# Optimization experiments

Hardware: AMD Instinct MI355X
Metric: run time of the kernel (lower is better)

Reference implementation:

```python
import jax, jax.numpy as jnp
import numpy as np

HEADS = 8
DIM_HEAD = 64
SCALE = DIM_HEAD ** -0.5


def setup_inputs() -> dict:
    key = jax.random.key(0)
    ks = jax.random.split(key, 5)
    B, N, M, D = 8, 1024, 1024, 512
    inner = HEADS * DIM_HEAD  # 512
    return {
        "x": jax.random.normal(ks[0], (B, N, D), dtype=jnp.float32),
        "context": jax.random.normal(ks[1], (B, M, D), dtype=jnp.float32),
        "Wq": jax.random.normal(ks[2], (D, inner), dtype=jnp.float32) * (D ** -0.5),
        "Wkv": jax.random.normal(ks[3], (D, 2 * inner), dtype=jnp.float32) * (D ** -0.5),
        "Wo": jax.random.normal(ks[4], (inner, D), dtype=jnp.float32) * (inner ** -0.5),
        "bo": jnp.zeros((D,), dtype=jnp.float32),
    }


def reference(x, context, Wq, Wkv, Wo, bo):
    B, N, D = x.shape
    M = context.shape[1]
    q = x @ Wq                      # [B, N, inner]
    kv = context @ Wkv              # [B, M, 2*inner]
    k, v = jnp.split(kv, 2, axis=-1)
    # b n (h d) -> b h n d
    split_heads = lambda t: t.reshape(t.shape[0], t.shape[1], HEADS, DIM_HEAD).transpose(0, 2, 1, 3)
    q, k, v = split_heads(q), split_heads(k), split_heads(v)
    dots = jnp.einsum('bhid,bhjd->bhij', q, k) * SCALE  # [B, H, N, M]
    attn = jax.nn.softmax(dots, axis=-1)
    out = jnp.einsum('bhij,bhjd->bhid', attn, v)        # [B, H, N, d]
    out = out.transpose(0, 2, 1, 3).reshape(B, N, HEADS * DIM_HEAD)
    return out @ Wo + bo            # [B, N, D]
```

## Files before the change

### kernel.cpp

```cpp
#include <hip/hip_runtime.h>
#include <stdint.h>

#define LOG2E 1.44269504088896340736f
#define QSCALE (0.125f * LOG2E)

typedef __bf16 bf16x8 __attribute__((ext_vector_type(8)));
typedef float floatx4 __attribute__((ext_vector_type(4)));

__device__ __forceinline__ unsigned short bfbits(float f) {
  __bf16 h = (__bf16)f;
  return __builtin_bit_cast(unsigned short, h);
}

__device__ __forceinline__ float fast_exp2(float x) {
#if __has_builtin(__builtin_amdgcn_exp2f)
  return __builtin_amdgcn_exp2f(x);
#else
  return exp2f(x);
#endif
}

__device__ __forceinline__ void gl2lds16(const void* g, void* l) {
  __builtin_amdgcn_global_load_lds((const __attribute__((address_space(1))) void*)g,
                                   (__attribute__((address_space(3))) void*)l, 16, 0, 0);
}

__global__ __launch_bounds__(256) void cvt2_f32_bf16(const float* __restrict__ a,
                                                     const float* __restrict__ b,
                                                     unsigned short* __restrict__ oa,
                                                     unsigned short* __restrict__ ob) {
  int blk = blockIdx.x;
  const float* in = blk < 4096 ? a : b;
  unsigned short* out = blk < 4096 ? oa : ob;
  int i = (((blk & 4095) * 256) + threadIdx.x) * 4;
  float4 v = *(const float4*)(in + i);
  unsigned long long pk = (unsigned long long)bfbits(v.x)
                        | ((unsigned long long)bfbits(v.y) << 16)
                        | ((unsigned long long)bfbits(v.z) << 32)
                        | ((unsigned long long)bfbits(v.w) << 48);
  *(unsigned long long*)(out + i) = pk;
}

__global__ __launch_bounds__(256) void transpose_cvt3(const float* __restrict__ w0,
                                                      const float* __restrict__ w1,
                                                      const float* __restrict__ w2,
                                                      unsigned short* __restrict__ o0,
                                                      unsigned short* __restrict__ o1,
                                                      unsigned short* __restrict__ o2) {
  __shared__ float tile[32][33];
  int z = blockIdx.z;
  const float* in = (z == 0) ? w0 : ((z == 1) ? w1 : w2);
  unsigned short* out = (z == 0) ? o0 : ((z == 1) ? o1 : o2);
  const int N = (z == 1) ? 1024 : 512;
  if (blockIdx.x * 32 >= N) return;
  const int K = 512;
  int k0 = blockIdx.y * 32, n0 = blockIdx.x * 32;
#pragma unroll
  for (int r = threadIdx.y; r < 32; r += 8)
    tile[r][threadIdx.x] = in[(long)(k0 + r) * N + n0 + threadIdx.x];
  __syncthreads();
#pragma unroll
  for (int r = threadIdx.y; r < 32; r += 8)
    out[(long)(n0 + r) * K + k0 + threadIdx.x] = bfbits(tile[threadIdx.x][r]);
}

template <int EPI, int BM>
__global__ __launch_bounds__(256)
void gemm_bf16(const unsigned short* __restrict__ A,
               const unsigned short* __restrict__ Bt,
               unsigned short* __restrict__ outA,
               unsigned short* __restrict__ outB,
               float* __restrict__ outF,
               const float* __restrict__ bias,
               int M, int N, int K)
{
  constexpr int IC = BM / 32;
  __shared__ unsigned short As[BM * 32];
  __shared__ unsigned short Bs[128 * 32];

  const int tid = threadIdx.x;
  const int wave = tid >> 6;
  const int lane = tid & 63;
  const int l15 = lane & 15;
  const int q4 = lane >> 4;
  const int wm = (wave & 1) * (BM / 2);
  const int wn = (wave >> 1) * 64;
  const long bm = (long)blockIdx.y * BM;
  const long bn = (long)blockIdx.x * 128;

  floatx4 acc[IC][4];
#pragma unroll
  for (int i = 0; i < IC; ++i)
#pragma unroll
    for (int j = 0; j < 4; ++j) { acc[i][j][0]=0.f; acc[i][j][1]=0.f; acc[i][j][2]=0.f; acc[i][j][3]=0.f; }

  for (int k0 = 0; k0 < K; k0 += 32) {
#pragma unroll
    for (int cc = 0; cc < BM / 64; ++cc) {
      int c = cc * 256 + tid;
      int r = c >> 2, kc = c & 3;
      gl2lds16(A + (bm + r) * (long)K + k0 + kc * 8, (char*)As + c * 16);
    }
#pragma unroll
    for (int cc = 0; cc < 2; ++cc) {
      int c = cc * 256 + tid;
      int r = c >> 2, kc = c & 3;
      gl2lds16(Bt + (bn + r) * (long)K + k0 + kc * 8, (char*)Bs + c * 16);
    }
    __syncthreads();
    bf16x8 af[IC], bfr[4];
#pragma unroll
    for (int i = 0; i < IC; ++i)
      af[i] = *(const bf16x8*)(As + (wm + i * 16 + l15) * 32 + q4 * 8);
#pragma unroll
    for (int j = 0; j < 4; ++j)
      bfr[j] = *(const bf16x8*)(Bs + (wn + j * 16 + l15) * 32 + q4 * 8);
#pragma unroll
    for (int i = 0; i < IC; ++i)
#pragma unroll
      for (int j = 0; j < 4; ++j)
        acc[i][j] = __builtin_amdgcn_mfma_f32_16x16x32_bf16(af[i], bfr[j], acc[i][j], 0, 0, 0);
    __syncthreads();
  }

#pragma unroll
  for (int i = 0; i < IC; ++i) {
#pragma unroll
    for (int j = 0; j < 4; ++j) {
      long col = bn + wn + j * 16 + l15;
      if (EPI == 1 && bn >= 512) {
        long h = (col - 512) >> 6, d = col & 63;
        long row0 = bm + wm + i * 16 + q4 * 4;
        long b = row0 >> 10, m0 = row0 & 1023;
        unsigned long long pk = (unsigned long long)bfbits(acc[i][j][0])
                              | ((unsigned long long)bfbits(acc[i][j][1]) << 16)
                              | ((unsigned long long)bfbits(acc[i][j][2]) << 32)
                              | ((unsigned long long)bfbits(acc[i][j][3]) << 48);
        *(unsigned long long*)(outB + ((b * 8 + h) * 64 + d) * 1024 + m0) = pk;
      } else {
#pragma unroll
        for (int r = 0; r < 4; ++r) {
          long row = bm + wm + i * 16 + q4 * 4 + r;
          float v = acc[i][j][r];
          if (EPI == 0) {
            long b = row >> 10, n = row & 1023;
            long h = col >> 6, d = col & 63;
            outA[((b * 8 + h) * 1024 + n) * 64 + d] = bfbits(v * QSCALE);
          } else if (EPI == 1) {
            long b = row >> 10, m = row & 1023;
            long h = col >> 6, d = col & 63;
            outA[((b * 8 + h) * 1024 + m) * 64 + d] = bfbits(v);
          } else {
            outF[row * (long)N + col] = v + bias[col];
          }
        }
      }
    }
  }
}

__global__ __launch_bounds__(256)
void attn_kernel(const unsigned short* __restrict__ Qb,
                 const unsigned short* __restrict__ Kb,
                 const unsigned short* __restrict__ Vt,
                 unsigned short* __restrict__ Ob)
{
  __shared__ unsigned short Ksm[2][4096];
  __shared__ unsigned short Vsm[2][4096];
  __shared__ unsigned short Psm[128 * 64];

  const int tid = threadIdx.x;
  const int wave = tid >> 6;
  const int lane = tid & 63;
  const int l15 = lane & 15;
  const int q4 = lane >> 4;
  const int bh = blockIdx.x;
  const int nb = blockIdx.y;

  const long qrow0 = (long)bh * 1024 + nb * 128 + wave * 32;

  bf16x8 qf[2][2];
#pragma unroll
  for (int i = 0; i < 2; ++i)
#pragma unroll
    for (int ks = 0; ks < 2; ++ks)
      qf[i][ks] = *(const bf16x8*)(Qb + (qrow0 + i * 16 + l15) * 64 + ks * 32 + q4 * 8);

  floatx4 acc[2][4];
#pragma unroll
  for (int i = 0; i < 2; ++i)
#pragma unroll
    for (int d = 0; d < 4; ++d) { acc[i][d][0]=0.f; acc[i][d][1]=0.f; acc[i][d][2]=0.f; acc[i][d][3]=0.f; }
  float suml[2][4];
#pragma unroll
  for (int i = 0; i < 2; ++i)
#pragma unroll
    for (int r = 0; r < 4; ++r) suml[i][r] = 0.0f;

  const unsigned short* Kbase = Kb + (long)bh * 65536;
  const unsigned short* Vbase = Vt + (long)bh * 65536;
  int koff[2], voff[2], lds16[2];
#pragma unroll
  for (int cc = 0; cc < 2; ++cc) {
    int c = cc * 256 + tid;
    int jrow = c >> 3;
    int cact = (c & 7) ^ (jrow & 7);
    koff[cc] = jrow * 64 + cact * 8;
    voff[cc] = jrow * 1024 + cact * 8;
    lds16[cc] = c * 16;
  }

#pragma unroll
  for (int cc = 0; cc < 2; ++cc) {
    gl2lds16(Kbase + koff[cc], (char*)Ksm[0] + lds16[cc]);
    gl2lds16(Vbase + voff[cc], (char*)Vsm[0] + lds16[cc]);
  }

  for (int t = 0; t < 16; ++t) {
    __syncthreads();
    const int cur = t & 1;
    if (t + 1 < 16) {
      const int nxt = cur ^ 1;
#pragma unroll
      for (int cc = 0; cc < 2; ++cc) {
        gl2lds16(Kbase + (t + 1) * 4096 + koff[cc], (char*)Ksm[nxt] + lds16[cc]);
        gl2lds16(Vbase + (t + 1) * 64 + voff[cc], (char*)Vsm[nxt] + lds16[cc]);
      }
    }

    floatx4 s[2][4];
#pragma unroll
    for (int i = 0; i < 2; ++i)
#pragma unroll
      for (int j = 0; j < 4; ++j) { s[i][j][0]=0.f; s[i][j][1]=0.f; s[i][j][2]=0.f; s[i][j][3]=0.f; }
#pragma unroll
    for (int ks = 0; ks < 2; ++ks) {
      bf16x8 kfr[4];
#pragma unroll
      for (int jn = 0; jn < 4; ++jn) {
        int j = jn * 16 + l15;
        int cact = (ks * 4 + q4) ^ (j & 7);
        kfr[jn] = *(const bf16x8*)(Ksm[cur] + j * 64 + cact * 8);
      }
#pragma unroll
      for (int i = 0; i < 2; ++i)
#pragma unroll
        for (int jn = 0; jn < 4; ++jn)
          s[i][jn] = __builtin_amdgcn_mfma_f32_16x16x32_bf16(qf[i][ks], kfr[jn], s[i][jn], 0, 0, 0);
    }

#pragma unroll
    for (int i = 0; i < 2; ++i) {
#pragma unroll
      for (int jn = 0; jn < 4; ++jn) {
        int colbase = jn * 16 + l15;
#pragma unroll
        for (int r = 0; r < 4; ++r) {
          float p = fast_exp2(s[i][jn][r]);
          suml[i][r] += p;
          int row = wave * 32 + i * 16 + q4 * 4 + r;
          int idx = row * 64 + (((colbase >> 3) ^ (row & 7)) << 3) + (colbase & 7);
          ((__bf16*)Psm)[idx] = (__bf16)p;
        }
      }
    }
    __asm__ volatile("s_waitcnt lgkmcnt(0)" ::: "memory");

#pragma unroll
    for (int ks = 0; ks < 2; ++ks) {
      bf16x8 pa[2], vb[4];
#pragma unroll
      for (int i = 0; i < 2; ++i) {
        int m = wave * 32 + i * 16 + l15;
        int cact = (ks * 4 + q4) ^ (m & 7);
        pa[i] = *(const bf16x8*)(Psm + m * 64 + cact * 8);
      }
#pragma unroll
      for (int dn = 0; dn < 4; ++dn) {
        int dd = dn * 16 + l15;
        int cact = (ks * 4 + q4) ^ (dd & 7);
        vb[dn] = *(const bf16x8*)(Vsm[cur] + dd * 64 + cact * 8);
      }
#pragma unroll
      for (int i = 0; i < 2; ++i)
#pragma unroll
        for (int dn = 0; dn < 4; ++dn)
          acc[i][dn] = __builtin_amdgcn_mfma_f32_16x16x32_bf16(pa[i], vb[dn], acc[i][dn], 0, 0, 0);
    }
  }

  const int b = bh >> 3, h = bh & 7;
#pragma unroll
  for (int i = 0; i < 2; ++i) {
    float inv[4];
#pragma unroll
    for (int r = 0; r < 4; ++r) {
      float l = suml[i][r];
#pragma unroll
      for (int off = 8; off >= 1; off >>= 1)
        l += __shfl_xor(l, off, 64);
      inv[r] = 1.0f / l;
    }
#pragma unroll
    for (int dn = 0; dn < 4; ++dn) {
#pragma unroll
      for (int r = 0; r < 4; ++r) {
        long row = (long)b * 1024 + nb * 128 + wave * 32 + i * 16 + q4 * 4 + r;
        long col = h * 64 + dn * 16 + l15;
        Ob[row * 512 + col] = bfbits(acc[i][dn][r] * inv[r]);
      }
    }
  }
}

extern "C" void kernel_launch(void* const* d_in, const int* in_sizes, int n_in,
                              void* d_out, int out_size, void* d_ws, size_t ws_size,
                              hipStream_t stream) {
  const float* x   = (const float*)d_in[0];
  const float* ctx = (const float*)d_in[1];
  const float* Wq  = (const float*)d_in[2];
  const float* Wkv = (const float*)d_in[3];
  const float* Wo  = (const float*)d_in[4];
  const float* bo  = (const float*)d_in[5];
  float* out = (float*)d_out;

  char* ws = (char*)d_ws;
  unsigned short* Xb   = (unsigned short*)(ws);
  unsigned short* Cb   = (unsigned short*)(ws + (8u  << 20));
  unsigned short* WqT  = (unsigned short*)(ws + (16u << 20));
  unsigned short* WkvT = (unsigned short*)(ws + (17u << 20));
  unsigned short* WoT  = (unsigned short*)(ws + (19u << 20));
  unsigned short* Qb   = (unsigned short*)(ws + (20u << 20));
  unsigned short* Kb   = (unsigned short*)(ws + (28u << 20));
  unsigned short* Vt   = (unsigned short*)(ws + (36u << 20));
  unsigned short* Ob   = (unsigned short*)(ws + (44u << 20));

  cvt2_f32_bf16<<<8192, 256, 0, stream>>>(x, ctx, Xb, Cb);
  transpose_cvt3<<<dim3(32, 16, 3), dim3(32, 8), 0, stream>>>(Wq, Wkv, Wo, WqT, WkvT, WoT);

  gemm_bf16<0, 64><<<dim3(4, 128), 256, 0, stream>>>(Xb, WqT, Qb, nullptr, nullptr, nullptr, 8192, 512, 512);
  gemm_bf16<1, 128><<<dim3(8, 64), 256, 0, stream>>>(Cb, WkvT, Kb, Vt, nullptr, nullptr, 8192, 1024, 512);
  attn_kernel<<<dim3(64, 8), 256, 0, stream>>>(Qb, Kb, Vt, Ob);
  gemm_bf16<2, 64><<<dim3(4, 128), 256, 0, stream>>>(Ob, WoT, nullptr, nullptr, out, bo, 8192, 512, 512);
}
```

Baseline: 174.0 us.

## Merge prep and projection kernels, halve attention tile, transpose S MFMA

Folds the two conversion kernels into one launch and the Q and KV projection GEMMs into one 1536-block launch, cutting launch count from six to four. The attention kernel now handles 64 query rows per block (16 per wave) and launches twice as many blocks, which gives more parallelism and less register pressure per wave. It computes S transposed (K as the A operand) so each lane holds four consecutive P values and writes them as one packed 8-byte LDS store instead of scalar bf16 stores. The row-sum reduction now needs only two shuffles plus a broadcast. In exchange, each K/V tile loaded into LDS is reused by fewer query rows, so K/V traffic per block rises.

New measurement: 162.4 us. -6.7%, faster.

```diff
diff --git a/kernel.cpp b/kernel.cpp
--- a/kernel.cpp
+++ b/kernel.cpp
@@ -25,81 +25,79 @@
                                    (__attribute__((address_space(3))) void*)l, 16, 0, 0);
 }
 
-__global__ __launch_bounds__(256) void cvt2_f32_bf16(const float* __restrict__ a,
-                                                     const float* __restrict__ b,
-                                                     unsigned short* __restrict__ oa,
-                                                     unsigned short* __restrict__ ob) {
+__global__ __launch_bounds__(256)
+void prep_kernel(const float* __restrict__ x, const float* __restrict__ ctx,
+                 const float* __restrict__ Wq, const float* __restrict__ Wkv,
+                 const float* __restrict__ Wo,
+                 unsigned short* __restrict__ Xb, unsigned short* __restrict__ Cb,
+                 unsigned short* __restrict__ WqT, unsigned short* __restrict__ WkvT,
+                 unsigned short* __restrict__ WoT) {
   int blk = blockIdx.x;
-  const float* in = blk < 4096 ? a : b;
-  unsigned short* out = blk < 4096 ? oa : ob;
-  int i = (((blk & 4095) * 256) + threadIdx.x) * 4;
-  float4 v = *(const float4*)(in + i);
-  unsigned long long pk = (unsigned long long)bfbits(v.x)
-                        | ((unsigned long long)bfbits(v.y) << 16)
-                        | ((unsigned long long)bfbits(v.z) << 32)
-                        | ((unsigned long long)bfbits(v.w) << 48);
-  *(unsigned long long*)(out + i) = pk;
-}
-
-__global__ __launch_bounds__(256) void transpose_cvt3(const float* __restrict__ w0,
-                                                      const float* __restrict__ w1,
-                                                      const float* __restrict__ w2,
-                                                      unsigned short* __restrict__ o0,
-                                                      unsigned short* __restrict__ o1,
-                                                      unsigned short* __restrict__ o2) {
-  __shared__ float tile[32][33];
-  int z = blockIdx.z;
-  const float* in = (z == 0) ? w0 : ((z == 1) ? w1 : w2);
-  unsigned short* out = (z == 0) ? o0 : ((z == 1) ? o1 : o2);
-  const int N = (z == 1) ? 1024 : 512;
-  if (blockIdx.x * 32 >= N) return;
-  const int K = 512;
-  int k0 = blockIdx.y * 32, n0 = blockIdx.x * 32;
-#pragma unroll
-  for (int r = threadIdx.y; r < 32; r += 8)
-    tile[r][threadIdx.x] = in[(long)(k0 + r) * N + n0 + threadIdx.x];
-  __syncthreads();
-#pragma unroll
-  for (int r = threadIdx.y; r < 32; r += 8)
-    out[(long)(n0 + r) * K + k0 + threadIdx.x] = bfbits(tile[threadIdx.x][r]);
-}
-
-template <int EPI, int BM>
+  int tid = threadIdx.x;
+  if (blk < 8192) {
+    const float* in = blk < 4096 ? x : ctx;
+    unsigned short* out = blk < 4096 ? Xb : Cb;
+    int i = (((blk & 4095) * 256) + tid) * 4;
+    float4 v = *(const float4*)(in + i);
+    unsigned long long pk = (unsigned long long)bfbits(v.x)
+                          | ((unsigned long long)bfbits(v.y) << 16)
+                          | ((unsigned long long)bfbits(v.z) << 32)
+                          | ((unsigned long long)bfbits(v.w) << 48);
+    *(unsigned long long*)(out + i) = pk;
+  } else {
+    __shared__ float tile[32][33];
+    int t = blk - 8192;
+    const float* in; unsigned short* out; int N; int tb;
+    if (t < 256)      { in = Wq;  out = WqT;  N = 512;  tb = t; }
+    else if (t < 768) { in = Wkv; out = WkvT; N = 1024; tb = t - 256; }
+    else              { in = Wo;  out = WoT;  N = 512;  tb = t - 768; }
+    const int K = 512;
+    int nbx = N / 32;
+    int n0 = (tb % nbx) * 32, k0 = (tb / nbx) * 32;
+    int tx = tid & 31, ty = tid >> 5;
+#pragma unroll
+    for (int r = ty; r < 32; r += 8)
+      tile[r][tx] = in[(long)(k0 + r) * N + n0 + tx];
+    __syncthreads();
+#pragma unroll
+    for (int r = ty; r < 32; r += 8)
+      out[(long)(n0 + r) * K + k0 + tx] = bfbits(tile[tx][r]);
+  }
+}
+
 __global__ __launch_bounds__(256)
-void gemm_bf16(const unsigned short* __restrict__ A,
-               const unsigned short* __restrict__ Bt,
-               unsigned short* __restrict__ outA,
-               unsigned short* __restrict__ outB,
-               float* __restrict__ outF,
-               const float* __restrict__ bias,
-               int M, int N, int K)
-{
-  constexpr int IC = BM / 32;
-  __shared__ unsigned short As[BM * 32];
+void proj_gemm(const unsigned short* __restrict__ Xb, const unsigned short* __restrict__ Cb,
+               const unsigned short* __restrict__ WqT, const unsigned short* __restrict__ WkvT,
+               unsigned short* __restrict__ Qb, unsigned short* __restrict__ Kb,
+               unsigned short* __restrict__ Vt) {
+  __shared__ unsigned short As[64 * 32];
   __shared__ unsigned short Bs[128 * 32];
+
+  int idx = blockIdx.x;
+  const unsigned short* A; const unsigned short* Bt;
+  long bm, bn; int role;
+  if (idx < 512) { role = 0; A = Xb; Bt = WqT;  bn = (long)(idx & 3) * 128; bm = (long)(idx >> 2) * 64; }
+  else { idx -= 512; role = 1; A = Cb; Bt = WkvT; bn = (long)(idx & 7) * 128; bm = (long)(idx >> 3) * 64; }
 
   const int tid = threadIdx.x;
   const int wave = tid >> 6;
   const int lane = tid & 63;
   const int l15 = lane & 15;
   const int q4 = lane >> 4;
-  const int wm = (wave & 1) * (BM / 2);
+  const int wm = (wave & 1) * 32;
   const int wn = (wave >> 1) * 64;
-  const long bm = (long)blockIdx.y * BM;
-  const long bn = (long)blockIdx.x * 128;
-
-  floatx4 acc[IC][4];
-#pragma unroll
-  for (int i = 0; i < IC; ++i)
+  const int K = 512;
+
+  floatx4 acc[2][4];
+#pragma unroll
+  for (int i = 0; i < 2; ++i)
 #pragma unroll
     for (int j = 0; j < 4; ++j) { acc[i][j][0]=0.f; acc[i][j][1]=0.f; acc[i][j][2]=0.f; acc[i][j][3]=0.f; }
 
   for (int k0 = 0; k0 < K; k0 += 32) {
-#pragma unroll
-    for (int cc = 0; cc < BM / 64; ++cc) {
-      int c = cc * 256 + tid;
-      int r = c >> 2, kc = c & 3;
-      gl2lds16(A + (bm + r) * (long)K + k0 + kc * 8, (char*)As + c * 16);
+    {
+      int r = tid >> 2, kc = tid & 3;
+      gl2lds16(A + (bm + r) * (long)K + k0 + kc * 8, (char*)As + tid * 16);
     }
 #pragma unroll
     for (int cc = 0; cc < 2; ++cc) {
@@ -108,15 +106,15 @@
       gl2lds16(Bt + (bn + r) * (long)K + k0 + kc * 8, (char*)Bs + c * 16);
     }
     __syncthreads();
-    bf16x8 af[IC], bfr[4];
-#pragma unroll
-    for (int i = 0; i < IC; ++i)
+    bf16x8 af[2], bfr[4];
+#pragma unroll
+    for (int i = 0; i < 2; ++i)
       af[i] = *(const bf16x8*)(As + (wm + i * 16 + l15) * 32 + q4 * 8);
 #pragma unroll
     for (int j = 0; j < 4; ++j)
       bfr[j] = *(const bf16x8*)(Bs + (wn + j * 16 + l15) * 32 + q4 * 8);
 #pragma unroll
-    for (int i = 0; i < IC; ++i)
+    for (int i = 0; i < 2; ++i)
 #pragma unroll
       for (int j = 0; j < 4; ++j)
         acc[i][j] = __builtin_amdgcn_mfma_f32_16x16x32_bf16(af[i], bfr[j], acc[i][j], 0, 0, 0);
@@ -124,11 +122,11 @@
   }
 
 #pragma unroll
-  for (int i = 0; i < IC; ++i) {
+  for (int i = 0; i < 2; ++i) {
 #pragma unroll
     for (int j = 0; j < 4; ++j) {
       long col = bn + wn + j * 16 + l15;
-      if (EPI == 1 && bn >= 512) {
+      if (role == 1 && col >= 512) {
         long h = (col - 512) >> 6, d = col & 63;
         long row0 = bm + wm + i * 16 + q4 * 4;
         long b = row0 >> 10, m0 = row0 & 1023;
@@ -136,23 +134,16 @@
                               | ((unsigned long long)bfbits(acc[i][j][1]) << 16)
                               | ((unsigned long long)bfbits(acc[i][j][2]) << 32)
                               | ((unsigned long long)bfbits(acc[i][j][3]) << 48);
-        *(unsigned long long*)(outB + ((b * 8 + h) * 64 + d) * 1024 + m0) = pk;
+        *(unsigned long long*)(Vt + ((b * 8 + h) * 64 + d) * 1024 + m0) = pk;
       } else {
+        long h = col >> 6, d = col & 63;
 #pragma unroll
         for (int r = 0; r < 4; ++r) {
           long row = bm + wm + i * 16 + q4 * 4 + r;
+          long b = row >> 10, n = row & 1023;
           float v = acc[i][j][r];
-          if (EPI == 0) {
-            long b = row >> 10, n = row & 1023;
-            long h = col >> 6, d = col & 63;
-            outA[((b * 8 + h) * 1024 + n) * 64 + d] = bfbits(v * QSCALE);
-          } else if (EPI == 1) {
-            long b = row >> 10, m = row & 1023;
-            long h = col >> 6, d = col & 63;
-            outA[((b * 8 + h) * 1024 + m) * 64 + d] = bfbits(v);
-          } else {
-            outF[row * (long)N + col] = v + bias[col];
-          }
+          if (role == 0) Qb[((b * 8 + h) * 1024 + n) * 64 + d] = bfbits(v * QSCALE);
+          else           Kb[((b * 8 + h) * 1024 + n) * 64 + d] = bfbits(v);
         }
       }
     }
@@ -167,7 +158,7 @@
 {
   __shared__ unsigned short Ksm[2][4096];
   __shared__ unsigned short Vsm[2][4096];
-  __shared__ unsigned short Psm[128 * 64];
+  __shared__ unsigned short Psm[64 * 64];
 
   const int tid = threadIdx.x;
   const int wave = tid >> 6;
@@ -177,25 +168,15 @@
   const int bh = blockIdx.x;
   const int nb = blockIdx.y;
 
-  const long qrow0 = (long)bh * 1024 + nb * 128 + wave * 32;
-
-  bf16x8 qf[2][2];
-#pragma unroll
-  for (int i = 0; i < 2; ++i)
-#pragma unroll
-    for (int ks = 0; ks < 2; ++ks)
-      qf[i][ks] = *(const bf16x8*)(Qb + (qrow0 + i * 16 + l15) * 64 + ks * 32 + q4 * 8);
-
-  floatx4 acc[2][4];
-#pragma unroll
-  for (int i = 0; i < 2; ++i)
-#pragma unroll
-    for (int d = 0; d < 4; ++d) { acc[i][d][0]=0.f; acc[i][d][1]=0.f; acc[i][d][2]=0.f; acc[i][d][3]=0.f; }
-  float suml[2][4];
-#pragma unroll
-  for (int i = 0; i < 2; ++i)
-#pragma unroll
-    for (int r = 0; r < 4; ++r) suml[i][r] = 0.0f;
+  bf16x8 qf[2];
+#pragma unroll
+  for (int ks = 0; ks < 2; ++ks)
+    qf[ks] = *(const bf16x8*)(Qb + ((long)bh * 1024 + nb * 64 + wave * 16 + l15) * 64 + ks * 32 + q4 * 8);
+
+  floatx4 acc[4];
+#pragma unroll
+  for (int d = 0; d < 4; ++d) { acc[d][0]=0.f; acc[d][1]=0.f; acc[d][2]=0.f; acc[d][3]=0.f; }
+  float suml = 0.0f;
 
   const unsigned short* Kbase = Kb + (long)bh * 65536;
   const unsigned short* Vbase = Vt + (long)bh * 65536;
@@ -209,13 +190,14 @@
     voff[cc] = jrow * 1024 + cact * 8;
     lds16[cc] = c * 16;
   }
-
 #pragma unroll
   for (int cc = 0; cc < 2; ++cc) {
     gl2lds16(Kbase + koff[cc], (char*)Ksm[0] + lds16[cc]);
     gl2lds16(Vbase + voff[cc], (char*)Vsm[0] + lds16[cc]);
   }
 
+  const int prow = wave * 16 + l15;
+
   for (int t = 0; t < 16; ++t) {
     __syncthreads();
     const int cur = t & 1;
@@ -228,11 +210,9 @@
       }
     }
 
-    floatx4 s[2][4];
-#pragma unroll
-    for (int i = 0; i < 2; ++i)
-#pragma unroll
-      for (int j = 0; j < 4; ++j) { s[i][j][0]=0.f; s[i][j][1]=0.f; s[i][j][2]=0.f; s[i][j][3]=0.f; }
+    floatx4 st[4];
+#pragma unroll
+    for (int jn = 0; jn < 4; ++jn) { st[jn][0]=0.f; st[jn][1]=0.f; st[jn][2]=0.f; st[jn][3]=0.f; }
 #pragma unroll
     for (int ks = 0; ks < 2; ++ks) {
       bf16x8 kfr[4];
@@ -243,38 +223,30 @@
         kfr[jn] = *(const bf16x8*)(Ksm[cur] + j * 64 + cact * 8);
       }
 #pragma unroll
-      for (int i = 0; i < 2; ++i)
-#pragma unroll
-        for (int jn = 0; jn < 4; ++jn)
-          s[i][jn] = __builtin_amdgcn_mfma_f32_16x16x32_bf16(qf[i][ks], kfr[jn], s[i][jn], 0, 0, 0);
-    }
-
-#pragma unroll
-    for (int i = 0; i < 2; ++i) {
-#pragma unroll
-      for (int jn = 0; jn < 4; ++jn) {
-        int colbase = jn * 16 + l15;
-#pragma unroll
-        for (int r = 0; r < 4; ++r) {
-          float p = fast_exp2(s[i][jn][r]);
-          suml[i][r] += p;
-          int row = wave * 32 + i * 16 + q4 * 4 + r;
-          int idx = row * 64 + (((colbase >> 3) ^ (row & 7)) << 3) + (colbase & 7);
-          ((__bf16*)Psm)[idx] = (__bf16)p;
-        }
-      }
+      for (int jn = 0; jn < 4; ++jn)
+        st[jn] = __builtin_amdgcn_mfma_f32_16x16x32_bf16(kfr[jn], qf[ks], st[jn], 0, 0, 0);
+    }
+
+#pragma unroll
+    for (int jn = 0; jn < 4; ++jn) {
+      float p0 = fast_exp2(st[jn][0]);
+      float p1 = fast_exp2(st[jn][1]);
+      float p2 = fast_exp2(st[jn][2]);
+      float p3 = fast_exp2(st[jn][3]);
+      suml += (p0 + p1) + (p2 + p3);
+      unsigned long long pk = (unsigned long long)bfbits(p0)
+                            | ((unsigned long long)bfbits(p1) << 16)
+                            | ((unsigned long long)bfbits(p2) << 32)
+                            | ((unsigned long long)bfbits(p3) << 48);
+      int ch8 = (jn * 2 + (q4 >> 1)) ^ (prow & 7);
+      *(unsigned long long*)(Psm + prow * 64 + ch8 * 8 + (q4 & 1) * 4) = pk;
     }
     __asm__ volatile("s_waitcnt lgkmcnt(0)" ::: "memory");
 
 #pragma unroll
     for (int ks = 0; ks < 2; ++ks) {
-      bf16x8 pa[2], vb[4];
-#pragma unroll
-      for (int i = 0; i < 2; ++i) {
-        int m = wave * 32 + i * 16 + l15;
-        int cact = (ks * 4 + q4) ^ (m & 7);
-        pa[i] = *(const bf16x8*)(Psm + m * 64 + cact * 8);
-      }
+      bf16x8 pa = *(const bf16x8*)(Psm + prow * 64 + (((ks * 4 + q4) ^ (prow & 7)) * 8));
+      bf16x8 vb[4];
 #pragma unroll
       for (int dn = 0; dn < 4; ++dn) {
         int dd = dn * 16 + l15;
@@ -282,32 +254,92 @@
         vb[dn] = *(const bf16x8*)(Vsm[cur] + dd * 64 + cact * 8);
       }
 #pragma unroll
-      for (int i = 0; i < 2; ++i)
-#pragma unroll
-        for (int dn = 0; dn < 4; ++dn)
-          acc[i][dn] = __builtin_amdgcn_mfma_f32_16x16x32_bf16(pa[i], vb[dn], acc[i][dn], 0, 0, 0);
-    }
-  }
+      for (int dn = 0; dn < 4; ++dn)
+        acc[dn] = __builtin_amdgcn_mfma_f32_16x16x32_bf16(pa, vb[dn], acc[dn], 0, 0, 0);
+    }
+  }
+
+  float l = suml;
+  l += __shfl_xor(l, 16, 64);
+  l += __shfl_xor(l, 32, 64);
+  float inv = 1.0f / l;
+  float invr[4];
+#pragma unroll
+  for (int r = 0; r < 4; ++r) invr[r] = __shfl(inv, q4 * 4 + r, 64);
 
   const int b = bh >> 3, h = bh & 7;
 #pragma unroll
+  for (int dn = 0; dn < 4; ++dn) {
+#pragma unroll
+    for (int r = 0; r < 4; ++r) {
+      long row = (long)b * 1024 + nb * 64 + wave * 16 + q4 * 4 + r;
+      long col = h * 64 + dn * 16 + l15;
+      Ob[row * 512 + col] = bfbits(acc[dn][r] * invr[r]);
+    }
+  }
+}
+
+__global__ __launch_bounds__(256)
+void out_gemm(const unsigned short* __restrict__ A,
+              const unsigned short* __restrict__ Bt,
+              float* __restrict__ outF, const float* __restrict__ bias) {
+  __shared__ unsigned short As[64 * 32];
+  __shared__ unsigned short Bs[128 * 32];
+
+  const int tid = threadIdx.x;
+  const int wave = tid >> 6;
+  const int lane = tid & 63;
+  const int l15 = lane & 15;
+  const int q4 = lane >> 4;
+  const int wm = (wave & 1) * 32;
+  const int wn = (wave >> 1) * 64;
+  const long bm = (long)blockIdx.y * 64;
+  const long bn = (long)blockIdx.x * 128;
+  const int K = 512, N = 512;
+
+  floatx4 acc[2][4];
+#pragma unroll
+  for (int i = 0; i < 2; ++i)
+#pragma unroll
+    for (int j = 0; j < 4; ++j) { acc[i][j][0]=0.f; acc[i][j][1]=0.f; acc[i][j][2]=0.f; acc[i][j][3]=0.f; }
+
+  for (int k0 = 0; k0 < K; k0 += 32) {
+    {
+      int r = tid >> 2, kc = tid & 3;
+      gl2lds16(A + (bm + r) * (long)K + k0 + kc * 8, (char*)As + tid * 16);
+    }
+#pragma unroll
+    for (int cc = 0; cc < 2; ++cc) {
+      int c = cc * 256 + tid;
+      int r = c >> 2, kc = c & 3;
+      gl2lds16(Bt + (bn + r) * (long)K + k0 + kc * 8, (char*)Bs + c * 16);
+    }
+    __syncthreads();
+    bf16x8 af[2], bfr[4];
+#pragma unroll
+    for (int i = 0; i < 2; ++i)
+      af[i] = *(const bf16x8*)(As + (wm + i * 16 + l15) * 32 + q4 * 8);
+#pragma unroll
+    for (int j = 0; j < 4; ++j)
+      bfr[j] = *(const bf16x8*)(Bs + (wn + j * 16 + l15) * 32 + q4 * 8);
+#pragma unroll
+    for (int i = 0; i < 2; ++i)
+#pragma unroll
+      for (int j = 0; j < 4; ++j)
+        acc[i][j] = __builtin_amdgcn_mfma_f32_16x16x32_bf16(af[i], bfr[j], acc[i][j], 0, 0, 0);
+    __syncthreads();
+  }
+
+#pragma unroll
   for (int i = 0; i < 2; ++i) {
-    float inv[4];
-#pragma unroll
-    for (int r = 0; r < 4; ++r) {
-      float l = suml[i][r];
-#pragma unroll
-      for (int off = 8; off >= 1; off >>= 1)
-        l += __shfl_xor(l, off, 64);
-      inv[r] = 1.0f / l;
-    }
-#pragma unroll
-    for (int dn = 0; dn < 4; ++dn) {
+#pragma unroll
+    for (int j = 0; j < 4; ++j) {
+      long col = bn + wn + j * 16 + l15;
+      float bv = bias[col];
 #pragma unroll
       for (int r = 0; r < 4; ++r) {
-        long row = (long)b * 1024 + nb * 128 + wave * 32 + i * 16 + q4 * 4 + r;
-        long col = h * 64 + dn * 16 + l15;
-        Ob[row * 512 + col] = bfbits(acc[i][dn][r] * inv[r]);
+        long row = bm + wm + i * 16 + q4 * 4 + r;
+        outF[row * (long)N + col] = acc[i][j][r] + bv;
       }
     }
   }
@@ -335,11 +367,8 @@
   unsigned short* Vt   = (unsigned short*)(ws + (36u << 20));
   unsigned short* Ob   = (unsigned short*)(ws + (44u << 20));
 
-  cvt2_f32_bf16<<<8192, 256, 0, stream>>>(x, ctx, Xb, Cb);
-  transpose_cvt3<<<dim3(32, 16, 3), dim3(32, 8), 0, stream>>>(Wq, Wkv, Wo, WqT, WkvT, WoT);
-
-  gemm_bf16<0, 64><<<dim3(4, 128), 256, 0, stream>>>(Xb, WqT, Qb, nullptr, nullptr, nullptr, 8192, 512, 512);
-  gemm_bf16<1, 128><<<dim3(8, 64), 256, 0, stream>>>(Cb, WkvT, Kb, Vt, nullptr, nullptr, 8192, 1024, 512);
-  attn_kernel<<<dim3(64, 8), 256, 0, stream>>>(Qb, Kb, Vt, Ob);
-  gemm_bf16<2, 64><<<dim3(4, 128), 256, 0, stream>>>(Ob, WoT, nullptr, nullptr, out, bo, 8192, 512, 512);
-}
+  prep_kernel<<<9216, 256, 0, stream>>>(x, ctx, Wq, Wkv, Wo, Xb, Cb, WqT, WkvT, WoT);
+  proj_gemm<<<1536, 256, 0, stream>>>(Xb, Cb, WqT, WkvT, Qb, Kb, Vt);
+  attn_kernel<<<dim3(64, 16), 256, 0, stream>>>(Qb, Kb, Vt, Ob);
+  out_gemm<<<dim3(4, 128), 256, 0, stream>>>(Ob, WoT, out, bo);
+}
```
